# Kernel tuning notes

Measured on AMD Instinct MI355X. Metric: run time of the kernel, lower is better.

The kernel has to match this reference:

```python
import jax, jax.numpy as jnp
import numpy as np

B, H, L, D = 16, 8, 128, 64
SCALE = jnp.float32(np.sqrt(D))
NEG = jnp.float32(-1e9)


def setup_inputs() -> dict:
    key = jax.random.key(0)
    kq, kk, kv, km = jax.random.split(key, 4)
    Q = jax.random.normal(kq, (B, H, L, D), dtype=jnp.float32)
    K = jax.random.normal(kk, (H, B, L, D), dtype=jnp.float32)
    V = jax.random.normal(kv, (H, B, L, D), dtype=jnp.float32)
    mask = jax.random.randint(km, (B, 1, 1, L, L), 0, 2, dtype=jnp.int32)
    return {"Q": Q, "K": K, "V": V, "mask": mask}


def reference(Q, K, V, mask):
    # Cross-sample (intersample) attention:
    # scores[b,h,c,i,j] = <Q[b,h,i,:], K[h,c,j,:]> / sqrt(D)  -> (B,H,B,L,L)
    scores = jnp.einsum('bhid,hcjd->bhcij', Q, K) / SCALE
    scores = jnp.where(mask == 0, NEG, scores)
    attn_weights = jax.nn.softmax(scores, axis=-1)  # (B,H,B,L,L)
    # output[b,h,c,i,:] = sum_j w[b,h,c,i,j] * V[h,c,j,:]  -> (B,H,B,L,D)
    output = jnp.einsum('bhcij,hcjd->bhcid', attn_weights, V)
    return (output, attn_weights)
```

## Files before the change

kernel.cpp:

```cpp
#include <hip/hip_runtime.h>
#include <hip/hip_bf16.h>

typedef float  f32x4  __attribute__((ext_vector_type(4)));
typedef __bf16 bf16x8 __attribute__((ext_vector_type(8)));
typedef __bf16 bf16x2 __attribute__((ext_vector_type(2)));

#define MFMA16(A,B,C) __builtin_amdgcn_mfma_f32_16x16x32_bf16((A),(B),(C),0,0,0)

constexpr int BN = 16, HN = 8, LN = 128, DN = 64;
constexpr size_t OUT0 = (size_t)BN * HN * BN * LN * DN;

__device__ __forceinline__ void load8_split(const float* __restrict__ p, float scale,
                                            bf16x8& hi, bf16x8& lo) {
  float f[8];
  *(float4*)&f[0] = *(const float4*)(p);
  *(float4*)&f[4] = *(const float4*)(p + 4);
#pragma unroll
  for (int i = 0; i < 8; ++i) {
    float x = f[i] * scale;
    __bf16 h = (__bf16)x;
    hi[i] = h;
    lo[i] = (__bf16)(x - (float)h);
  }
}

__device__ __forceinline__ void load8_hi(const float* __restrict__ p, bf16x8& hi) {
  float f[8];
  *(float4*)&f[0] = *(const float4*)(p);
  *(float4*)&f[4] = *(const float4*)(p + 4);
#pragma unroll
  for (int i = 0; i < 8; ++i) hi[i] = (__bf16)f[i];
}

__device__ __forceinline__ void lds8_split(const float* p, bf16x8& hi, bf16x8& lo) {
  float f[8];
  *(float4*)&f[0] = *(const float4*)(p);
  *(float4*)&f[4] = *(const float4*)(p + 4);
#pragma unroll
  for (int i = 0; i < 8; ++i) {
    __bf16 h = (__bf16)f[i];
    hi[i] = h;
    lo[i] = (__bf16)(f[i] - (float)h);
  }
}

__global__ __launch_bounds__(256, 3) void isa_attn_kernel(
    const float* __restrict__ Q, const float* __restrict__ K,
    const float* __restrict__ V, const int* __restrict__ M,
    float* __restrict__ out)
{
  __shared__ __bf16 VT[DN][136];
  __shared__ float P[LN][68];

  const int bid = blockIdx.x;
  const int b = bid >> 7;
  const int h = (bid >> 4) & 7;
  const int c = bid & 15;

  const float* Qp = Q + (size_t)(b * HN + h) * (LN * DN);
  const float* Kp = K + (size_t)(h * BN + c) * (LN * DN);
  const float* Vp = V + (size_t)(h * BN + c) * (LN * DN);
  const int*   Mp = M + (size_t)b * (LN * LN);
  float* Op = out + (size_t)bid * (LN * DN);
  float* Wp = out + OUT0 + (size_t)bid * (LN * LN);

  const int t    = threadIdx.x;
  const int lane = t & 63;
  const int wave = t >> 6;
  const int quad = lane >> 4;
  const int l16  = lane & 15;
  const int row0 = wave * 32;

#pragma unroll
  for (int it = 0; it < 4; ++it) {
    int idx = t + it * 256;
    int j2  = idx >> 4;
    int d0  = (idx & 15) * 4;
    float4 a = *(const float4*)(Vp + (2 * j2) * DN + d0);
    float4 bb = *(const float4*)(Vp + (2 * j2 + 1) * DN + d0);
    const float* af = (const float*)&a;
    const float* bf = (const float*)&bb;
#pragma unroll
    for (int w = 0; w < 4; ++w)
      *(bf16x2*)&VT[d0 + w][2 * j2] = (bf16x2){(__bf16)af[w], (__bf16)bf[w]};
  }

  bf16x8 qhi[2][2], qlo[2][2];
#pragma unroll
  for (int rt = 0; rt < 2; ++rt)
#pragma unroll
    for (int kt = 0; kt < 2; ++kt)
      load8_split(Qp + (row0 + rt * 16 + l16) * DN + kt * 32 + quad * 8, 0.125f,
                  qhi[rt][kt], qlo[rt][kt]);

  f32x4 acc[2][8];
#pragma unroll
  for (int rt = 0; rt < 2; ++rt)
#pragma unroll
    for (int ct = 0; ct < 8; ++ct)
      acc[rt][ct] = (f32x4){0.f, 0.f, 0.f, 0.f};

#pragma unroll
  for (int ct = 0; ct < 8; ++ct) {
#pragma unroll
    for (int kt = 0; kt < 2; ++kt) {
      bf16x8 kh;
      load8_hi(Kp + (ct * 16 + l16) * DN + kt * 32 + quad * 8, kh);
#pragma unroll
      for (int rt = 0; rt < 2; ++rt) {
        acc[rt][ct] = MFMA16(qhi[rt][kt], kh, acc[rt][ct]);
        acc[rt][ct] = MFMA16(qlo[rt][kt], kh, acc[rt][ct]);
      }
    }
  }

#pragma unroll
  for (int rt = 0; rt < 2; ++rt) {
#pragma unroll
    for (int r = 0; r < 4; ++r) {
      int row = row0 + rt * 16 + quad * 4 + r;
      const int* mrow = Mp + (size_t)row * LN + l16;
      float*     wrow = Wp + (size_t)row * LN + l16;
      float mf[8];
#pragma unroll
      for (int ct = 0; ct < 8; ++ct) mf[ct] = (float)mrow[ct * 16];
      float mx = -3.0e38f;
#pragma unroll
      for (int ct = 0; ct < 8; ++ct) mx = fmaxf(mx, acc[rt][ct][r]);
      mx = fmaxf(mx, __shfl_xor(mx, 1));
      mx = fmaxf(mx, __shfl_xor(mx, 2));
      mx = fmaxf(mx, __shfl_xor(mx, 4));
      mx = fmaxf(mx, __shfl_xor(mx, 8));
      float s[8];
      float sum = 0.f;
#pragma unroll
      for (int ct = 0; ct < 8; ++ct) {
        s[ct] = __expf(acc[rt][ct][r] - mx) * mf[ct];
        sum += s[ct];
      }
      sum += __shfl_xor(sum, 1);
      sum += __shfl_xor(sum, 2);
      sum += __shfl_xor(sum, 4);
      sum += __shfl_xor(sum, 8);
      float inv = __builtin_amdgcn_rcpf(sum);
      inv = inv * (2.0f - sum * inv);
#pragma unroll
      for (int ct = 0; ct < 8; ++ct) {
        float w = s[ct] * inv;
        acc[rt][ct][r] = w;
        wrow[ct * 16] = w;
      }
    }
  }

  __syncthreads();

  f32x4 oacc[2][4];
#pragma unroll
  for (int rt = 0; rt < 2; ++rt)
#pragma unroll
    for (int nt = 0; nt < 4; ++nt)
      oacc[rt][nt] = (f32x4){0.f, 0.f, 0.f, 0.f};

#pragma unroll
  for (int half = 0; half < 2; ++half) {
#pragma unroll
    for (int rt = 0; rt < 2; ++rt)
#pragma unroll
      for (int c4 = 0; c4 < 4; ++c4)
#pragma unroll
        for (int r = 0; r < 4; ++r)
          P[row0 + rt * 16 + quad * 4 + r][c4 * 16 + l16] = acc[rt][half * 4 + c4][r];

#pragma unroll
    for (int jt = 0; jt < 2; ++jt) {
      bf16x8 phi[2], plo[2];
#pragma unroll
      for (int rt = 0; rt < 2; ++rt)
        lds8_split(&P[row0 + rt * 16 + l16][jt * 32 + quad * 8], phi[rt], plo[rt]);
#pragma unroll
      for (int nt = 0; nt < 4; ++nt) {
        bf16x8 vh = *(const bf16x8*)&VT[nt * 16 + l16][half * 64 + jt * 32 + quad * 8];
#pragma unroll
        for (int rt = 0; rt < 2; ++rt) {
          oacc[rt][nt] = MFMA16(phi[rt], vh, oacc[rt][nt]);
          oacc[rt][nt] = MFMA16(plo[rt], vh, oacc[rt][nt]);
        }
      }
    }
  }

#pragma unroll
  for (int rt = 0; rt < 2; ++rt)
#pragma unroll
    for (int nt = 0; nt < 4; ++nt)
#pragma unroll
      for (int r = 0; r < 4; ++r)
        Op[(row0 + rt * 16 + quad * 4 + r) * DN + nt * 16 + l16] = oacc[rt][nt][r];
}

extern "C" void kernel_launch(void* const* d_in, const int* in_sizes, int n_in,
                              void* d_out, int out_size, void* d_ws, size_t ws_size,
                              hipStream_t stream) {
  const float* Q = (const float*)d_in[0];
  const float* K = (const float*)d_in[1];
  const float* V = (const float*)d_in[2];
  const int*   M = (const int*)d_in[3];
  isa_attn_kernel<<<dim3(BN * HN * BN), dim3(256), 0, stream>>>(Q, K, V, M, (float*)d_out);
}
```

Measured before the change: 249.3 us.

## Stage K in LDS, coalesce output stores via LDS, remap blocks for locality

Converts K to bf16 once into shared memory instead of each wave reloading it from global memory. Restages the attention weights and the output tile through a narrower LDS buffer so they are written with row-contiguous float4 stores rather than strided scalar stores. Also remaps block indices so co-resident blocks share h and c, aiming at better L2 reuse of K and V, and rewrites the V transpose to use wider bf16x8 LDS writes. This adds LDS traffic and an extra barrier.

```diff
diff --git a/kernel.cpp b/kernel.cpp
--- a/kernel.cpp
+++ b/kernel.cpp
@@ -3,12 +3,15 @@
 
 typedef float  f32x4  __attribute__((ext_vector_type(4)));
 typedef __bf16 bf16x8 __attribute__((ext_vector_type(8)));
-typedef __bf16 bf16x2 __attribute__((ext_vector_type(2)));
 
 #define MFMA16(A,B,C) __builtin_amdgcn_mfma_f32_16x16x32_bf16((A),(B),(C),0,0,0)
 
 constexpr int BN = 16, HN = 8, LN = 128, DN = 64;
 constexpr size_t OUT0 = (size_t)BN * HN * BN * LN * DN;
+
+constexpr int KTS = 72;
+constexpr int VTS = 136;
+constexpr int PS  = 36;
 
 __device__ __forceinline__ void load8_split(const float* __restrict__ p, float scale,
                                             bf16x8& hi, bf16x8& lo) {
@@ -24,14 +27,6 @@
   }
 }
 
-__device__ __forceinline__ void load8_hi(const float* __restrict__ p, bf16x8& hi) {
-  float f[8];
-  *(float4*)&f[0] = *(const float4*)(p);
-  *(float4*)&f[4] = *(const float4*)(p + 4);
-#pragma unroll
-  for (int i = 0; i < 8; ++i) hi[i] = (__bf16)f[i];
-}
-
 __device__ __forceinline__ void lds8_split(const float* p, bf16x8& hi, bf16x8& lo) {
   float f[8];
   *(float4*)&f[0] = *(const float4*)(p);
@@ -49,40 +44,58 @@
     const float* __restrict__ V, const int* __restrict__ M,
     float* __restrict__ out)
 {
-  __shared__ __bf16 VT[DN][136];
-  __shared__ float P[LN][68];
+  __shared__ __bf16 KT[LN * KTS];
+  __shared__ __bf16 VT[DN * VTS];
+  __shared__ float  P [LN * PS];
 
   const int bid = blockIdx.x;
-  const int b = bid >> 7;
-  const int h = (bid >> 4) & 7;
-  const int c = bid & 15;
+  const int w = (bid & 7) * 256 + (bid >> 3);
+  const int h = w >> 8;
+  const int c = (w >> 4) & 15;
+  const int b = w & 15;
 
   const float* Qp = Q + (size_t)(b * HN + h) * (LN * DN);
   const float* Kp = K + (size_t)(h * BN + c) * (LN * DN);
   const float* Vp = V + (size_t)(h * BN + c) * (LN * DN);
   const int*   Mp = M + (size_t)b * (LN * LN);
-  float* Op = out + (size_t)bid * (LN * DN);
-  float* Wp = out + OUT0 + (size_t)bid * (LN * LN);
+  float* Op = out + (size_t)((b * HN + h) * BN + c) * (LN * DN);
+  float* Wp = out + OUT0 + (size_t)((b * HN + h) * BN + c) * (LN * LN);
 
   const int t    = threadIdx.x;
   const int lane = t & 63;
-  const int wave = t >> 6;
+  const int wid  = t >> 6;
   const int quad = lane >> 4;
   const int l16  = lane & 15;
-  const int row0 = wave * 32;
+  const int row0 = wid * 32;
 
 #pragma unroll
   for (int it = 0; it < 4; ++it) {
     int idx = t + it * 256;
-    int j2  = idx >> 4;
-    int d0  = (idx & 15) * 4;
-    float4 a = *(const float4*)(Vp + (2 * j2) * DN + d0);
-    float4 bb = *(const float4*)(Vp + (2 * j2 + 1) * DN + d0);
-    const float* af = (const float*)&a;
-    const float* bf = (const float*)&bb;
-#pragma unroll
-    for (int w = 0; w < 4; ++w)
-      *(bf16x2*)&VT[d0 + w][2 * j2] = (bf16x2){(__bf16)af[w], (__bf16)bf[w]};
+    int n  = idx >> 3;
+    int k0 = (idx & 7) * 8;
+    float4 a0 = *(const float4*)(Kp + n * DN + k0);
+    float4 a1 = *(const float4*)(Kp + n * DN + k0 + 4);
+    bf16x8 kk;
+    kk[0] = (__bf16)a0.x; kk[1] = (__bf16)a0.y; kk[2] = (__bf16)a0.z; kk[3] = (__bf16)a0.w;
+    kk[4] = (__bf16)a1.x; kk[5] = (__bf16)a1.y; kk[6] = (__bf16)a1.z; kk[7] = (__bf16)a1.w;
+    *(bf16x8*)&KT[n * KTS + k0] = kk;
+  }
+
+  {
+    int j8 = t >> 4;
+    int d0 = (t & 15) * 4;
+    float4 vv[8];
+#pragma unroll
+    for (int r = 0; r < 8; ++r)
+      vv[r] = *(const float4*)(Vp + (j8 * 8 + r) * DN + d0);
+#pragma unroll
+    for (int dw = 0; dw < 4; ++dw) {
+      bf16x8 col;
+#pragma unroll
+      for (int r = 0; r < 8; ++r)
+        col[r] = (__bf16)(((const float*)&vv[r])[dw]);
+      *(bf16x8*)&VT[(d0 + dw) * VTS + j8 * 8] = col;
+    }
   }
 
   bf16x8 qhi[2][2], qlo[2][2];
@@ -93,6 +106,8 @@
       load8_split(Qp + (row0 + rt * 16 + l16) * DN + kt * 32 + quad * 8, 0.125f,
                   qhi[rt][kt], qlo[rt][kt]);
 
+  __syncthreads();
+
   f32x4 acc[2][8];
 #pragma unroll
   for (int rt = 0; rt < 2; ++rt)
@@ -104,8 +119,7 @@
   for (int ct = 0; ct < 8; ++ct) {
 #pragma unroll
     for (int kt = 0; kt < 2; ++kt) {
-      bf16x8 kh;
-      load8_hi(Kp + (ct * 16 + l16) * DN + kt * 32 + quad * 8, kh);
+      bf16x8 kh = *(const bf16x8*)&KT[(ct * 16 + l16) * KTS + kt * 32 + quad * 8];
 #pragma unroll
       for (int rt = 0; rt < 2; ++rt) {
         acc[rt][ct] = MFMA16(qhi[rt][kt], kh, acc[rt][ct]);
@@ -120,7 +134,6 @@
     for (int r = 0; r < 4; ++r) {
       int row = row0 + rt * 16 + quad * 4 + r;
       const int* mrow = Mp + (size_t)row * LN + l16;
-      float*     wrow = Wp + (size_t)row * LN + l16;
       float mf[8];
 #pragma unroll
       for (int ct = 0; ct < 8; ++ct) mf[ct] = (float)mrow[ct * 16];
@@ -145,15 +158,9 @@
       float inv = __builtin_amdgcn_rcpf(sum);
       inv = inv * (2.0f - sum * inv);
 #pragma unroll
-      for (int ct = 0; ct < 8; ++ct) {
-        float w = s[ct] * inv;
-        acc[rt][ct][r] = w;
-        wrow[ct * 16] = w;
-      }
-    }
-  }
-
-  __syncthreads();
+      for (int ct = 0; ct < 8; ++ct) acc[rt][ct][r] = s[ct] * inv;
+    }
+  }
 
   f32x4 oacc[2][4];
 #pragma unroll
@@ -163,40 +170,59 @@
       oacc[rt][nt] = (f32x4){0.f, 0.f, 0.f, 0.f};
 
 #pragma unroll
-  for (int half = 0; half < 2; ++half) {
+  for (int qu = 0; qu < 4; ++qu) {
 #pragma unroll
     for (int rt = 0; rt < 2; ++rt)
 #pragma unroll
-      for (int c4 = 0; c4 < 4; ++c4)
+      for (int cc = 0; cc < 2; ++cc)
 #pragma unroll
         for (int r = 0; r < 4; ++r)
-          P[row0 + rt * 16 + quad * 4 + r][c4 * 16 + l16] = acc[rt][half * 4 + c4][r];
-
-#pragma unroll
-    for (int jt = 0; jt < 2; ++jt) {
-      bf16x8 phi[2], plo[2];
-#pragma unroll
-      for (int rt = 0; rt < 2; ++rt)
-        lds8_split(&P[row0 + rt * 16 + l16][jt * 32 + quad * 8], phi[rt], plo[rt]);
-#pragma unroll
-      for (int nt = 0; nt < 4; ++nt) {
-        bf16x8 vh = *(const bf16x8*)&VT[nt * 16 + l16][half * 64 + jt * 32 + quad * 8];
-#pragma unroll
-        for (int rt = 0; rt < 2; ++rt) {
-          oacc[rt][nt] = MFMA16(phi[rt], vh, oacc[rt][nt]);
-          oacc[rt][nt] = MFMA16(plo[rt], vh, oacc[rt][nt]);
-        }
+          P[(row0 + rt * 16 + quad * 4 + r) * PS + cc * 16 + l16] =
+              acc[rt][qu * 2 + cc][r];
+
+#pragma unroll
+    for (int e = 0; e < 4; ++e) {
+      int idx = e * 64 + lane;
+      int rl  = idx >> 3;
+      int c4  = idx & 7;
+      float4 v = *(const float4*)&P[(row0 + rl) * PS + c4 * 4];
+      *(float4*)&Wp[(size_t)(row0 + rl) * LN + qu * 32 + c4 * 4] = v;
+    }
+
+    bf16x8 phi[2], plo[2];
+#pragma unroll
+    for (int rt = 0; rt < 2; ++rt)
+      lds8_split(&P[(row0 + rt * 16 + l16) * PS + quad * 8], phi[rt], plo[rt]);
+#pragma unroll
+    for (int nt = 0; nt < 4; ++nt) {
+      bf16x8 vh = *(const bf16x8*)&VT[(nt * 16 + l16) * VTS + qu * 32 + quad * 8];
+#pragma unroll
+      for (int rt = 0; rt < 2; ++rt) {
+        oacc[rt][nt] = MFMA16(phi[rt], vh, oacc[rt][nt]);
+        oacc[rt][nt] = MFMA16(plo[rt], vh, oacc[rt][nt]);
       }
     }
   }
 
 #pragma unroll
-  for (int rt = 0; rt < 2; ++rt)
-#pragma unroll
-    for (int nt = 0; nt < 4; ++nt)
-#pragma unroll
-      for (int r = 0; r < 4; ++r)
-        Op[(row0 + rt * 16 + quad * 4 + r) * DN + nt * 16 + l16] = oacc[rt][nt][r];
+  for (int hf = 0; hf < 2; ++hf) {
+#pragma unroll
+    for (int rt = 0; rt < 2; ++rt)
+#pragma unroll
+      for (int nn = 0; nn < 2; ++nn)
+#pragma unroll
+        for (int r = 0; r < 4; ++r)
+          P[(row0 + rt * 16 + quad * 4 + r) * PS + nn * 16 + l16] =
+              oacc[rt][hf * 2 + nn][r];
+#pragma unroll
+    for (int e = 0; e < 4; ++e) {
+      int idx = e * 64 + lane;
+      int rl  = idx >> 3;
+      int c4  = idx & 7;
+      float4 v = *(const float4*)&P[(row0 + rl) * PS + c4 * 4];
+      *(float4*)&Op[(size_t)(row0 + rl) * DN + hf * 32 + c4 * 4] = v;
+    }
+  }
 }
 
 extern "C" void kernel_launch(void* const* d_in, const int* in_sizes, int n_in,
```

New measurement: 238.4 us. 4.4% less time.
